# Performance work log

Hardware: AMD Instinct MI355X
Metric: run time of the kernel (lower is better)

## Reference

```python
import jax, jax.numpy as jnp
import numpy as np

BS, LATENT, HID, MAXLEN = 128, 512, 1024, 512

def setup_inputs() -> dict:
    key = jax.random.key(0)
    ks = jax.random.split(key, 12)
    s = 1.0 / np.sqrt(HID)  # pytorch default LSTM init scale
    inp = {}
    inp["decoder_input"] = jax.random.normal(ks[0], (BS, LATENT), jnp.float32)
    inp["lengths"] = jax.random.randint(ks[1], (BS,), 0, MAXLEN)
    # bidirectional single-layer LSTM params (gate order i,f,g,o; combined bias = b_ih+b_hh)
    inp["Wih_f"] = jax.random.uniform(ks[2], (4 * HID, LATENT), jnp.float32, -s, s)
    inp["Whh_f"] = jax.random.uniform(ks[3], (4 * HID, HID), jnp.float32, -s, s)
    inp["b_f"] = jax.random.uniform(ks[4], (4 * HID,), jnp.float32, -s, s)
    inp["Wih_b"] = jax.random.uniform(ks[5], (4 * HID, LATENT), jnp.float32, -s, s)
    inp["Whh_b"] = jax.random.uniform(ks[6], (4 * HID, HID), jnp.float32, -s, s)
    inp["b_b"] = jax.random.uniform(ks[7], (4 * HID,), jnp.float32, -s, s)
    # out: Linear(hidden -> latent); fc1: Linear(2*hidden -> 1)
    inp["W_out"] = jax.random.uniform(ks[8], (LATENT, HID), jnp.float32, -s, s)
    inp["b_out"] = jax.random.uniform(ks[9], (LATENT,), jnp.float32, -s, s)
    inp["W_fc1"] = jax.random.uniform(ks[10], (1, 2 * HID), jnp.float32, -s, s)
    inp["b_fc1"] = jax.random.uniform(ks[11], (1,), jnp.float32, -s, s)
    return inp

def _lstm_cell(x, h, c, Wih, Whh, b):
    z = x @ Wih.T + h @ Whh.T + b  # (bs, 4H)
    i, f, g, o = jnp.split(z, 4, axis=-1)
    c2 = jax.nn.sigmoid(f) * c + jax.nn.sigmoid(i) * jnp.tanh(g)
    h2 = jax.nn.sigmoid(o) * jnp.tanh(c2)
    return h2, c2

def reference(decoder_input, lengths, Wih_f, Whh_f, b_f, Wih_b, Whh_b, b_b,
              W_out, b_out, W_fc1, b_fc1):
    max_len = int(jnp.max(lengths))  # static decode length
    bs = decoder_input.shape[0]
    h0 = jnp.zeros((bs, HID), decoder_input.dtype)

    def step(carry, _):
        x, hf, cf, hb, cb = carry
        # bidirectional LSTM over a length-1 sequence = two cells on same input
        hf, cf = _lstm_cell(x, hf, cf, Wih_f, Whh_f, b_f)
        hb, cb = _lstm_cell(x, hb, cb, Wih_b, Whh_b, b_b)
        out_t = jnp.concatenate([hf, hb], axis=-1)  # (bs, 2H)
        # next input = out(h_n[-1]) i.e. backward-direction hidden
        x_next = hb @ W_out.T + b_out
        return (x_next, hf, cf, hb, cb), out_t

    carry0 = (decoder_input, h0, h0, h0, h0)
    _, outs = jax.lax.scan(step, carry0, xs=None, length=max_len)  # (T, bs, 2H)
    x = jnp.transpose(outs, (1, 0, 2))  # (bs, T, 2H)
    x = jax.nn.relu(x)
    return x @ W_fc1.T + b_fc1  # (bs, T, 1)
```

## Files before the change

kernel.cpp:

```cpp
#include <hip/hip_runtime.h>
#include <math.h>

typedef unsigned short u16;
typedef __attribute__((ext_vector_type(8))) short short8;
typedef __attribute__((ext_vector_type(4))) float f32x4;

__device__ __forceinline__ float sigm(float x) { return 1.0f / (1.0f + expf(-x)); }

__device__ __forceinline__ u16 f2bf(float x) {
    union { float f; unsigned u; } v; v.f = x;
    unsigned r = v.u + 0x7fffu + ((v.u >> 16) & 1u);
    return (u16)(r >> 16);
}
__device__ __forceinline__ float bf2f(u16 h) {
    union { unsigned u; float f; } v; v.u = ((unsigned)h) << 16;
    return v.f;
}
__device__ __forceinline__ f32x4 mfma16(short8 a, short8 b, f32x4 c) {
    return __builtin_amdgcn_mfma_f32_16x16x32_bf16(a, b, c, 0, 0, 0);
}
__device__ __forceinline__ void gl_lds16(const void* g, void* l) {
    __builtin_amdgcn_global_load_lds(
        (const __attribute__((address_space(1))) unsigned int*)g,
        (__attribute__((address_space(3))) unsigned int*)l, 16, 0, 0);
}
__device__ __forceinline__ int swz(int c) { return (c ^ (c >> 2)) & 3; }

__device__ __forceinline__ short8 ld_sc(const u16* p) {
    short8 r;
    asm volatile("global_load_dwordx4 %0, %1, off sc0 sc1"
                 : "=v"(r) : "v"(p) : "memory");
    return r;
}

__device__ __forceinline__ void grid_barrier(unsigned* cnt, unsigned* gen,
                                             unsigned nb, unsigned inst) {
    __syncthreads();
    if (threadIdx.x == 0) {
        const unsigned a = __hip_atomic_fetch_add(cnt, 1u, __ATOMIC_RELAXED,
                                                  __HIP_MEMORY_SCOPE_AGENT);
        if (a == nb * (inst + 1u) - 1u) {
            __hip_atomic_store(gen, inst + 1u, __ATOMIC_RELAXED,
                               __HIP_MEMORY_SCOPE_AGENT);
        } else {
            while (__hip_atomic_load(gen, __ATOMIC_RELAXED,
                                     __HIP_MEMORY_SCOPE_AGENT) < inst + 1u)
                __builtin_amdgcn_s_sleep(2);
        }
    }
    __syncthreads();
}

#define FENCE() asm volatile("" ::: "memory")

#define STAGE_W(kk, buf)                                                      \
    do {                                                                      \
        gl_lds16(Wsrc + sA + (kk), sm + (buf) * 8192 + lds0);                 \
        gl_lds16(Wsrc + sB + (kk), sm + (buf) * 8192 + lds1);                 \
    } while (0)

#define LOAD_A(kk, AH_, AL_)                                                  \
    do {                                                                      \
        _Pragma("unroll") for (int ks_ = 0; ks_ < 2; ++ks_) {                 \
            AH_[ks_] = ld_sc(Ah + aoff + (kk) + ks_ * 32);                    \
            AL_[ks_] = ld_sc(Al + aoff + (kk) + ks_ * 32);                    \
        }                                                                     \
    } while (0)

#define COMPUTE(bix, AH_, AL_, cix)                                           \
    do {                                                                      \
        const char* bb_ = sm + (bix) * 8192;                                  \
        _Pragma("unroll") for (int ks_ = 0; ks_ < 2; ++ks_) {                 \
            short8 bh_[2], bl_[2];                                            \
            _Pragma("unroll") for (int nt_ = 0; nt_ < 2; ++nt_) {             \
                const int col_ = nt_ * 16 + l15;                              \
                const int off_ = ks_ * 2048 + col_ * 64 + ((quad ^ swz(col_)) * 16); \
                bh_[nt_] = *(const short8*)(bb_ + off_);                      \
                bl_[nt_] = *(const short8*)(bb_ + 4096 + off_);               \
            }                                                                 \
            _Pragma("unroll") for (int nt_ = 0; nt_ < 2; ++nt_) {             \
                acc[nt_] = mfma16(AH_[ks_], bh_[nt_], acc[nt_]);              \
                acc[nt_] = mfma16(AL_[ks_], bh_[nt_], acc[nt_]);              \
                acc[nt_] = mfma16(AH_[ks_], bl_[nt_], acc[nt_]);              \
            }                                                                 \
        }                                                                     \
        if (fc1w) {                                                           \
            const int kb_ = (cix) * 64 + quad * 8;                            \
            _Pragma("unroll") for (int ks_ = 0; ks_ < 2; ++ks_) {             \
                const float* wp_ = smWf + kb_ + ks_ * 32;                     \
                const f32x4 w0_ = *(const f32x4*)(wp_);                       \
                const f32x4 w1_ = *(const f32x4*)(wp_ + 4);                   \
                const short8 hv_ = AH_[ks_];                                  \
                const short8 lv_ = AL_[ks_];                                  \
                _Pragma("unroll") for (int e_ = 0; e_ < 8; ++e_) {            \
                    const float v_ = bf2f((u16)hv_[e_]) + bf2f((u16)lv_[e_]); \
                    const float wv_ = (e_ < 4) ? w0_[e_] : w1_[e_ - 4];       \
                    fsum = fmaf(fmaxf(v_, 0.0f), wv_, fsum);                  \
                }                                                             \
            }                                                                 \
        }                                                                     \
    } while (0)

#define ITER(cc, BC, BS, AHU, ALU, AHL, ALL)                                  \
    do {                                                                      \
        asm volatile("s_waitcnt vmcnt(12)" ::: "memory");                     \
        __builtin_amdgcn_sched_barrier(0);                                    \
        __builtin_amdgcn_s_barrier();                                         \
        FENCE();                                                              \
        STAGE_W(((cc) + 3) * 64, BS);                                         \
        FENCE();                                                              \
        LOAD_A(((cc) + 3) * 64, AHL, ALL);                                    \
        COMPUTE(BC, AHU, ALU, (cc));                                          \
    } while (0)

__global__ __launch_bounds__(256, 2) void k_steps(
    u16* A0h, u16* A0l, u16* A1h, u16* A1l,
    const u16* __restrict__ WihH, const u16* __restrict__ WihL,
    const u16* __restrict__ WH, const u16* __restrict__ WL,
    const float* __restrict__ BR0, const float* __restrict__ BR1,
    const float* __restrict__ Wfc1, const float* __restrict__ bfc1,
    float* __restrict__ out,
    unsigned* barcnt, unsigned* bargen, int T)
{
    __shared__ __align__(16) char sm[32768];
    __shared__ __align__(16) char ze[9216];
    __shared__ __align__(16) float smWf[2048];

    const int tid = threadIdx.x, bid = blockIdx.x;
    const int w = tid >> 6, lane = tid & 63, l15 = lane & 15, quad = lane >> 4;
    const int dir = bid & 1;
    const int rest = bid >> 1;
    const int rowhalf = rest >> 7, colgrp = rest & 127;
    const int nbase = dir * 4096 + colgrp * 32;
    const int r0 = rowhalf * 64 + w * 16;
    const bool fc1b = (dir == 0) && (colgrp == 0);

    const int sp = w >> 1, skh = w & 1;
    const u16* Wsrc0 = sp ? WihL : WihH;
    const u16* WsrcN = sp ? WL : WH;
    size_t s0a, s0b, sNa, sNb;
    int lds0, lds1;
    {
        const int colA = 0 * 16 + (lane >> 2);
        const int colB = 1 * 16 + (lane >> 2);
        const int sa = (lane & 3) ^ swz(colA);
        const int sb = (lane & 3) ^ swz(colB);
        const size_t koffN = dir ? 1024 : 0;
        s0a = (size_t)(nbase + colA) * 512 + (size_t)(skh * 32 + sa * 8);
        s0b = (size_t)(nbase + colB) * 512 + (size_t)(skh * 32 + sb * 8);
        sNa = (size_t)(nbase + colA) * 2048 + koffN + (size_t)(skh * 32 + sa * 8);
        sNb = (size_t)(nbase + colB) * 2048 + koffN + (size_t)(skh * 32 + sb * 8);
        lds0 = sp * 4096 + skh * 2048;
        lds1 = lds0 + 1024;
    }

    const size_t abase = (size_t)(r0 + l15) * 2048 + (size_t)(quad * 8);
    const size_t aoffN = abase + (size_t)(dir ? 1024 : 0);

    const int ul = lane & 7;
    const f32x4 br0v = *(const f32x4*)(BR0 + nbase + ul * 4);
    const f32x4 br1v = *(const f32x4*)(BR1 + nbase + ul * 4);
    const float b1 = bfc1[0];
    float creg0 = 0.0f, creg1 = 0.0f;

    if (fc1b) {
        const f32x4 w0 = *(const f32x4*)(Wfc1 + tid * 8);
        const f32x4 w1 = *(const f32x4*)(Wfc1 + tid * 8 + 4);
        *(f32x4*)(smWf + tid * 8) = w0;
        *(f32x4*)(smWf + tid * 8 + 4) = w1;
    }
    asm volatile("s_waitcnt vmcnt(0) lgkmcnt(0)" ::: "memory");

    const unsigned nb = gridDim.x;

    for (int t = 0; t < T; ++t) {
        const int first = (t == 0);
        const u16* Ah = (t & 1) ? A1h : A0h;
        const u16* Al = (t & 1) ? A1l : A0l;
        u16* NAh = (t & 1) ? A0h : A1h;
        u16* NAl = (t & 1) ? A0l : A1l;
        const int nch = first ? 8 : (dir ? 16 : 32);
        const u16* Wsrc = first ? Wsrc0 : WsrcN;
        const size_t sA = first ? s0a : sNa;
        const size_t sB = first ? s0b : sNb;
        const size_t aoff = first ? abase : aoffN;
        const bool fc1w = fc1b && (t > 0);

        f32x4 acc[2] = {};
        short8 ah0[2], al0[2], ah1[2], al1[2];
        short8 ah2[2], al2[2], ah3[2], al3[2];
        float fsum = 0.0f;

        STAGE_W(0, 0);   FENCE(); LOAD_A(0, ah0, al0);   FENCE();
        STAGE_W(64, 1);  FENCE(); LOAD_A(64, ah1, al1);  FENCE();
        STAGE_W(128, 2); FENCE(); LOAD_A(128, ah2, al2); FENCE();

        for (int c = 0; c < nch; c += 4) {
            ITER(c + 0, 0, 3, ah0, al0, ah3, al3);
            ITER(c + 1, 1, 0, ah1, al1, ah0, al0);
            ITER(c + 2, 2, 1, ah2, al2, ah1, al1);
            ITER(c + 3, 3, 2, ah3, al3, ah2, al2);
        }
        asm volatile("s_waitcnt vmcnt(0)" ::: "memory");

        if (fc1w) {
            float v = fsum;
            v += __shfl_xor(v, 16);
            v += __shfl_xor(v, 32);
            if (lane < 16)
                out[(size_t)(r0 + l15) * T + (t - 1)] = v + b1;
        }

        char* zb = ze + w * 2304;
#pragma unroll
        for (int nt = 0; nt < 2; ++nt)
#pragma unroll
            for (int r = 0; r < 4; ++r)
                *(float*)(zb + (quad * 4 + r) * 144 + (nt * 16 + l15) * 4) = acc[nt][r];

        const f32x4 bv = first ? br0v : br1v;
#pragma unroll
        for (int p2 = 0; p2 < 2; ++p2) {
            const int ml = p2 * 8 + (lane >> 3);
            const f32x4 z = *(const f32x4*)(zb + ml * 144 + ul * 16);
            const float zi = z[0] + bv[0], zf = z[1] + bv[1];
            const float zg = z[2] + bv[2], zo = z[3] + bv[3];
            const float cold = p2 ? creg1 : creg0;
            const float c2 = sigm(zf) * cold + sigm(zi) * tanhf(zg);
            const float h2 = sigm(zo) * tanhf(c2);
            if (p2) creg1 = c2; else creg0 = c2;
            const u16 hh = f2bf(h2);
            const u16 hl = f2bf(h2 - bf2f(hh));
            const unsigned ohh = __shfl_xor((unsigned)hh, 1);
            const unsigned ohl = __shfl_xor((unsigned)hl, 1);
            if (!(lane & 1)) {
                const int u = colgrp * 8 + ul;
                const int m = r0 + ml;
                const size_t hidx = (size_t)m * 2048 + dir * 1024 + u;
                __hip_atomic_store((unsigned*)(NAh + hidx),
                                   (unsigned)hh | (ohh << 16),
                                   __ATOMIC_RELAXED, __HIP_MEMORY_SCOPE_AGENT);
                __hip_atomic_store((unsigned*)(NAl + hidx),
                                   (unsigned)hl | (ohl << 16),
                                   __ATOMIC_RELAXED, __HIP_MEMORY_SCOPE_AGENT);
            }
        }

        if (t + 1 < T)
            grid_barrier(barcnt, bargen, nb, (unsigned)t);
    }
}

__global__ __launch_bounds__(256) void k_tail(
    const u16* __restrict__ Ah, const u16* __restrict__ Al,
    const float* __restrict__ Wfc1, const float* __restrict__ bfc1,
    float* __restrict__ out, int T)
{
    __shared__ float red[256];
    const int m = blockIdx.x, tid = threadIdx.x;
    const size_t base = (size_t)m * 2048 + tid * 8;
    const short8 hv = *(const short8*)(Ah + base);
    const short8 lv = *(const short8*)(Al + base);
    float s = 0.0f;
#pragma unroll
    for (int e = 0; e < 8; ++e) {
        const float v = bf2f((u16)hv[e]) + bf2f((u16)lv[e]);
        s = fmaf(fmaxf(v, 0.0f), Wfc1[tid * 8 + e], s);
    }
    red[tid] = s;
    __syncthreads();
    for (int off = 128; off > 0; off >>= 1) {
        if (tid < off) red[tid] += red[tid + off];
        __syncthreads();
    }
    if (tid == 0) out[(size_t)m * T + T - 1] = red[0] + bfc1[0];
}

__global__ __launch_bounds__(256, 1) void k_fold(
    const u16* __restrict__ AH, const u16* __restrict__ AL,
    const u16* __restrict__ BH, const u16* __restrict__ BL,
    const float* __restrict__ Whh_b,
    u16* __restrict__ WH, u16* __restrict__ WL)
{
    const int tid = threadIdx.x, bid = blockIdx.x;
    const int w = tid >> 6, lane = tid & 63, l15 = lane & 15, quad = lane >> 4;
    const int bm = bid >> 4, bn = bid & 15;
    const int ar0 = bm * 64 + (w & 1) * 32;
    const int br0 = bn * 64 + (w >> 1) * 32;
    f32x4 acc[2][2] = {};
    for (int k0 = 0; k0 < 512; k0 += 32) {
        short8 a_h[2], a_l[2], b_h[2], b_l[2];
#pragma unroll
        for (int mt = 0; mt < 2; ++mt) {
            const size_t o = (size_t)(ar0 + mt * 16 + l15) * 512 + k0 + quad * 8;
            a_h[mt] = *(const short8*)(AH + o);
            a_l[mt] = *(const short8*)(AL + o);
        }
#pragma unroll
        for (int nt = 0; nt < 2; ++nt) {
            const size_t o = (size_t)(br0 + nt * 16 + l15) * 512 + k0 + quad * 8;
            b_h[nt] = *(const short8*)(BH + o);
            b_l[nt] = *(const short8*)(BL + o);
        }
#pragma unroll
        for (int mt = 0; mt < 2; ++mt)
#pragma unroll
            for (int nt = 0; nt < 2; ++nt) {
                acc[mt][nt] = mfma16(a_h[mt], b_h[nt], acc[mt][nt]);
                acc[mt][nt] = mfma16(a_l[mt], b_h[nt], acc[mt][nt]);
                acc[mt][nt] = mfma16(a_h[mt], b_l[nt], acc[mt][nt]);
            }
    }
#pragma unroll
    for (int mt = 0; mt < 2; ++mt)
#pragma unroll
        for (int nt = 0; nt < 2; ++nt)
#pragma unroll
            for (int r = 0; r < 4; ++r) {
                const int row = ar0 + mt * 16 + quad * 4 + r;
                const int j = br0 + nt * 16 + l15;
                float v = acc[mt][nt][r];
                if (row >= 4096)
                    v += Whh_b[(size_t)((row & 3) * 1024 + ((row & 4095) >> 2)) * 1024 + j];
                const size_t d = (size_t)row * 2048 + 1024 + j;
                const u16 hh = f2bf(v);
                WH[d] = hh;
                WL[d] = f2bf(v - bf2f(hh));
            }
}

__global__ __launch_bounds__(256) void k_prep(
    const float* __restrict__ dec,
    const float* __restrict__ Wih_f, const float* __restrict__ Whh_f,
    const float* __restrict__ b_f, const float* __restrict__ Wih_b,
    const float* __restrict__ b_b, const float* __restrict__ W_out,
    const float* __restrict__ b_out, const float* __restrict__ b_fc1,
    u16* __restrict__ WihH, u16* __restrict__ WihL,
    u16* __restrict__ WoTH, u16* __restrict__ WoTL,
    float* __restrict__ BR0, float* __restrict__ BR1,
    u16* __restrict__ A0h, u16* __restrict__ A0l,
    u16* __restrict__ WH, u16* __restrict__ WL,
    float* __restrict__ out, int out_size)
{
    const int t = blockIdx.x * 256 + threadIdx.x;
    if (t < 524288) {
        const int colp = t >> 6, kb = (t & 63) * 8;
        const int dir = colp >> 12, u = (colp & 4095) >> 2, g = colp & 3;
        const float* src = (dir ? Wih_b : Wih_f) + (size_t)(g * 1024 + u) * 512 + kb;
        const size_t d = (size_t)colp * 512 + kb;
#pragma unroll
        for (int j = 0; j < 8; ++j) {
            const float v = src[j];
            const u16 hh = f2bf(v);
            WihH[d + j] = hh; WihL[d + j] = f2bf(v - bf2f(hh));
        }
    } else if (t < 589824) {
        const int i = t - 524288, jc = i >> 6, lb = (i & 63) * 8;
#pragma unroll
        for (int jj = 0; jj < 8; ++jj) {
            const float v = W_out[(size_t)(lb + jj) * 1024 + jc];
            const size_t d = (size_t)jc * 512 + lb + jj;
            const u16 hh = f2bf(v);
            WoTH[d] = hh; WoTL[d] = f2bf(v - bf2f(hh));
        }
    } else if (t < 598016) {
        const int colp = t - 589824;
        const int dir = colp >> 12, u = (colp & 4095) >> 2, g = colp & 3;
        const float* Wih = dir ? Wih_b : Wih_f;
        const float s = (dir ? b_b : b_f)[g * 1024 + u];
        BR0[colp] = s;
        float dot = 0.0f;
        for (int l = 0; l < 512; ++l)
            dot += Wih[(size_t)(g * 1024 + u) * 512 + l] * b_out[l];
        BR1[colp] = s + dot;
    } else if (t < 606208) {
        const int i = t - 598016, m = i >> 6, kb = (i & 63) * 8;
#pragma unroll
        for (int j = 0; j < 8; ++j) {
            const float v = dec[(size_t)m * 512 + kb + j];
            const size_t d = (size_t)m * 2048 + kb + j;
            const u16 hh = f2bf(v);
            A0h[d] = hh; A0l[d] = f2bf(v - bf2f(hh));
        }
    } else if (t < 614400) {
        const int base = (t - 606208) * 8;
        const float b0 = b_fc1[0];
#pragma unroll
        for (int j = 0; j < 8; ++j)
            if (base + j < out_size) out[base + j] = b0;
    } else {
        const int i = t - 614400, colp = i >> 7, kb = (i & 127) * 8;
        const int u = colp >> 2, g = colp & 3;
        const float* src = Whh_f + (size_t)(g * 1024 + u) * 1024 + kb;
        const size_t d = (size_t)colp * 2048 + kb;
#pragma unroll
        for (int j = 0; j < 8; ++j) {
            const float v = src[j];
            const u16 hh = f2bf(v);
            WH[d + j] = hh; WL[d + j] = f2bf(v - bf2f(hh));
        }
    }
}

extern "C" void kernel_launch(void* const* d_in, const int* in_sizes, int n_in,
                              void* d_out, int out_size, void* d_ws, size_t ws_size,
                              hipStream_t stream) {
    const float* dec   = (const float*)d_in[0];
    const float* Wih_f = (const float*)d_in[2];
    const float* Whh_f = (const float*)d_in[3];
    const float* b_f   = (const float*)d_in[4];
    const float* Wih_b = (const float*)d_in[5];
    const float* Whh_b = (const float*)d_in[6];
    const float* b_b   = (const float*)d_in[7];
    const float* W_out = (const float*)d_in[8];
    const float* b_out = (const float*)d_in[9];
    const float* W_fc1 = (const float*)d_in[10];
    const float* b_fc1 = (const float*)d_in[11];
    float* out = (float*)d_out;

    char* ws = (char*)d_ws;
    u16* WH    = (u16*)(ws);
    u16* WL    = (u16*)(ws + 33554432);
    u16* WihH  = (u16*)(ws + 67108864);
    u16* WihL  = (u16*)(ws + 75497472);
    u16* WoTH  = (u16*)(ws + 83886080);
    u16* WoTL  = (u16*)(ws + 84934656);
    u16* A0h   = (u16*)(ws + 85983232);
    u16* A0l   = (u16*)(ws + 86507520);
    u16* A1h   = (u16*)(ws + 87031808);
    u16* A1l   = (u16*)(ws + 87556096);
    float* BR0 = (float*)(ws + 89128960);
    float* BR1 = (float*)(ws + 89161728);
    unsigned* barcnt = (unsigned*)(ws + 89194496);
    unsigned* bargen = (unsigned*)(ws + 89194624);

    k_prep<<<4448, 256, 0, stream>>>(dec, Wih_f, Whh_f, b_f, Wih_b, b_b,
                                     W_out, b_out, b_fc1,
                                     WihH, WihL, WoTH, WoTL, BR0, BR1,
                                     A0h, A0l, WH, WL, out, out_size);
    k_fold<<<2048, 256, 0, stream>>>(WihH, WihL, WoTH, WoTL, Whh_b, WH, WL);
    hipMemsetAsync(ws + 89194496, 0, 256, stream);

    const int T = out_size / 128;
    k_steps<<<512, 256, 0, stream>>>(A0h, A0l, A1h, A1l,
                                     WihH, WihL, WH, WL,
                                     BR0, BR1, W_fc1, b_fc1, out,
                                     barcnt, bargen, T);
    k_tail<<<128, 256, 0, stream>>>((T & 1) ? A1h : A0h, (T & 1) ? A1l : A0l,
                                    W_fc1, b_fc1, out, T);
}
```

Baseline: 21.63 ms.

## Use hierarchical grid barrier and double the K-chunk per pipeline stage

Replaces the flat single-counter grid barrier with a two-level barrier: groups of 8 blocks count on their own counters, and one representative per group bumps a root counter. This is meant to reduce atomic contention across 512 blocks at every timestep. It also doubles the K chunk per pipeline stage from 64 to 128, which halves the number of iterations and barriers per step. In exchange the LDS buffers double to 64KB, which may limit occupancy to one block per CU where launch bounds assume two. The z scratch buffer now aliases the staging buffer, with an added barrier to protect it, and the fc1 weights are read straight from global memory.

```diff
diff --git a/kernel.cpp b/kernel.cpp
--- a/kernel.cpp
+++ b/kernel.cpp
@@ -33,20 +33,24 @@
     return r;
 }
 
-__device__ __forceinline__ void grid_barrier(unsigned* cnt, unsigned* gen,
-                                             unsigned nb, unsigned inst) {
+__device__ __forceinline__ void grid_barrier(char* base, unsigned inst) {
     __syncthreads();
     if (threadIdx.x == 0) {
-        const unsigned a = __hip_atomic_fetch_add(cnt, 1u, __ATOMIC_RELAXED,
+        unsigned* root = (unsigned*)(base);
+        unsigned* gen  = (unsigned*)(base + 128);
+        unsigned* grp  = (unsigned*)(base + 256 + (blockIdx.x >> 3) * 128);
+        const unsigned a = __hip_atomic_fetch_add(grp, 1u, __ATOMIC_RELAXED,
                                                   __HIP_MEMORY_SCOPE_AGENT);
-        if (a == nb * (inst + 1u) - 1u) {
-            __hip_atomic_store(gen, inst + 1u, __ATOMIC_RELAXED,
-                               __HIP_MEMORY_SCOPE_AGENT);
-        } else {
-            while (__hip_atomic_load(gen, __ATOMIC_RELAXED,
-                                     __HIP_MEMORY_SCOPE_AGENT) < inst + 1u)
-                __builtin_amdgcn_s_sleep(2);
-        }
+        if (a == 8u * (inst + 1u) - 1u) {
+            const unsigned r = __hip_atomic_fetch_add(root, 1u, __ATOMIC_RELAXED,
+                                                      __HIP_MEMORY_SCOPE_AGENT);
+            if (r == 64u * (inst + 1u) - 1u)
+                __hip_atomic_store(gen, inst + 1u, __ATOMIC_RELAXED,
+                                   __HIP_MEMORY_SCOPE_AGENT);
+        }
+        while (__hip_atomic_load(gen, __ATOMIC_RELAXED,
+                                 __HIP_MEMORY_SCOPE_AGENT) < inst + 1u)
+            __builtin_amdgcn_s_sleep(2);
     }
     __syncthreads();
 }
@@ -55,43 +59,48 @@
 
 #define STAGE_W(kk, buf)                                                      \
     do {                                                                      \
-        gl_lds16(Wsrc + sA + (kk), sm + (buf) * 8192 + lds0);                 \
-        gl_lds16(Wsrc + sB + (kk), sm + (buf) * 8192 + lds1);                 \
+        _Pragma("unroll") for (int k64_ = 0; k64_ < 2; ++k64_) {              \
+            gl_lds16(Wsrc + sA + (kk) + k64_ * 64,                            \
+                     sm + (buf) * 16384 + ldsA + k64_ * 4096);                \
+            gl_lds16(Wsrc + sB + (kk) + k64_ * 64,                            \
+                     sm + (buf) * 16384 + ldsB + k64_ * 4096);                \
+        }                                                                     \
     } while (0)
 
 #define LOAD_A(kk, AH_, AL_)                                                  \
     do {                                                                      \
-        _Pragma("unroll") for (int ks_ = 0; ks_ < 2; ++ks_) {                 \
-            AH_[ks_] = ld_sc(Ah + aoff + (kk) + ks_ * 32);                    \
-            AL_[ks_] = ld_sc(Al + aoff + (kk) + ks_ * 32);                    \
+        _Pragma("unroll") for (int sb_ = 0; sb_ < 4; ++sb_) {                 \
+            AH_[sb_] = ld_sc(Ah + aoff + (kk) + sb_ * 32);                    \
+            AL_[sb_] = ld_sc(Al + aoff + (kk) + sb_ * 32);                    \
         }                                                                     \
     } while (0)
 
 #define COMPUTE(bix, AH_, AL_, cix)                                           \
     do {                                                                      \
-        const char* bb_ = sm + (bix) * 8192;                                  \
-        _Pragma("unroll") for (int ks_ = 0; ks_ < 2; ++ks_) {                 \
+        const char* bb_ = sm + (bix) * 16384;                                 \
+        _Pragma("unroll") for (int sb_ = 0; sb_ < 4; ++sb_) {                 \
+            const int k64_ = sb_ >> 1, ks_ = sb_ & 1;                         \
             short8 bh_[2], bl_[2];                                            \
             _Pragma("unroll") for (int nt_ = 0; nt_ < 2; ++nt_) {             \
                 const int col_ = nt_ * 16 + l15;                              \
-                const int off_ = ks_ * 2048 + col_ * 64 + ((quad ^ swz(col_)) * 16); \
+                const int off_ = k64_ * 4096 + ks_ * 2048 + col_ * 64 +       \
+                                 ((quad ^ swz(col_)) * 16);                   \
                 bh_[nt_] = *(const short8*)(bb_ + off_);                      \
-                bl_[nt_] = *(const short8*)(bb_ + 4096 + off_);               \
+                bl_[nt_] = *(const short8*)(bb_ + 8192 + off_);               \
             }                                                                 \
             _Pragma("unroll") for (int nt_ = 0; nt_ < 2; ++nt_) {             \
-                acc[nt_] = mfma16(AH_[ks_], bh_[nt_], acc[nt_]);              \
-                acc[nt_] = mfma16(AL_[ks_], bh_[nt_], acc[nt_]);              \
-                acc[nt_] = mfma16(AH_[ks_], bl_[nt_], acc[nt_]);              \
+                acc[nt_] = mfma16(AH_[sb_], bh_[nt_], acc[nt_]);              \
+                acc[nt_] = mfma16(AL_[sb_], bh_[nt_], acc[nt_]);              \
+                acc[nt_] = mfma16(AH_[sb_], bl_[nt_], acc[nt_]);              \
             }                                                                 \
         }                                                                     \
         if (fc1w) {                                                           \
-            const int kb_ = (cix) * 64 + quad * 8;                            \
-            _Pragma("unroll") for (int ks_ = 0; ks_ < 2; ++ks_) {             \
-                const float* wp_ = smWf + kb_ + ks_ * 32;                     \
+            _Pragma("unroll") for (int sb_ = 0; sb_ < 4; ++sb_) {             \
+                const float* wp_ = Wfc1 + (cix) * 128 + sb_ * 32 + quad * 8;  \
                 const f32x4 w0_ = *(const f32x4*)(wp_);                       \
                 const f32x4 w1_ = *(const f32x4*)(wp_ + 4);                   \
-                const short8 hv_ = AH_[ks_];                                  \
-                const short8 lv_ = AL_[ks_];                                  \
+                const short8 hv_ = AH_[sb_];                                  \
+                const short8 lv_ = AL_[sb_];                                  \
                 _Pragma("unroll") for (int e_ = 0; e_ < 8; ++e_) {            \
                     const float v_ = bf2f((u16)hv_[e_]) + bf2f((u16)lv_[e_]); \
                     const float wv_ = (e_ < 4) ? w0_[e_] : w1_[e_ - 4];       \
@@ -103,13 +112,13 @@
 
 #define ITER(cc, BC, BS, AHU, ALU, AHL, ALL)                                  \
     do {                                                                      \
-        asm volatile("s_waitcnt vmcnt(12)" ::: "memory");                     \
+        asm volatile("s_waitcnt vmcnt(24)" ::: "memory");                     \
         __builtin_amdgcn_sched_barrier(0);                                    \
         __builtin_amdgcn_s_barrier();                                         \
         FENCE();                                                              \
-        STAGE_W(((cc) + 3) * 64, BS);                                         \
+        STAGE_W(((cc) + 3) * 128, BS);                                        \
         FENCE();                                                              \
-        LOAD_A(((cc) + 3) * 64, AHL, ALL);                                    \
+        LOAD_A(((cc) + 3) * 128, AHL, ALL);                                   \
         COMPUTE(BC, AHU, ALU, (cc));                                          \
     } while (0)
 
@@ -119,12 +128,9 @@
     const u16* __restrict__ WH, const u16* __restrict__ WL,
     const float* __restrict__ BR0, const float* __restrict__ BR1,
     const float* __restrict__ Wfc1, const float* __restrict__ bfc1,
-    float* __restrict__ out,
-    unsigned* barcnt, unsigned* bargen, int T)
+    float* __restrict__ out, char* barbase, int T)
 {
-    __shared__ __align__(16) char sm[32768];
-    __shared__ __align__(16) char ze[9216];
-    __shared__ __align__(16) float smWf[2048];
+    __shared__ __align__(16) char sm[65536];
 
     const int tid = threadIdx.x, bid = blockIdx.x;
     const int w = tid >> 6, lane = tid & 63, l15 = lane & 15, quad = lane >> 4;
@@ -139,7 +145,7 @@
     const u16* Wsrc0 = sp ? WihL : WihH;
     const u16* WsrcN = sp ? WL : WH;
     size_t s0a, s0b, sNa, sNb;
-    int lds0, lds1;
+    int ldsA, ldsB;
     {
         const int colA = 0 * 16 + (lane >> 2);
         const int colB = 1 * 16 + (lane >> 2);
@@ -150,8 +156,8 @@
         s0b = (size_t)(nbase + colB) * 512 + (size_t)(skh * 32 + sb * 8);
         sNa = (size_t)(nbase + colA) * 2048 + koffN + (size_t)(skh * 32 + sa * 8);
         sNb = (size_t)(nbase + colB) * 2048 + koffN + (size_t)(skh * 32 + sb * 8);
-        lds0 = sp * 4096 + skh * 2048;
-        lds1 = lds0 + 1024;
+        ldsA = sp * 8192 + skh * 2048;
+        ldsB = ldsA + 1024;
     }
 
     const size_t abase = (size_t)(r0 + l15) * 2048 + (size_t)(quad * 8);
@@ -163,15 +169,7 @@
     const float b1 = bfc1[0];
     float creg0 = 0.0f, creg1 = 0.0f;
 
-    if (fc1b) {
-        const f32x4 w0 = *(const f32x4*)(Wfc1 + tid * 8);
-        const f32x4 w1 = *(const f32x4*)(Wfc1 + tid * 8 + 4);
-        *(f32x4*)(smWf + tid * 8) = w0;
-        *(f32x4*)(smWf + tid * 8 + 4) = w1;
-    }
     asm volatile("s_waitcnt vmcnt(0) lgkmcnt(0)" ::: "memory");
-
-    const unsigned nb = gridDim.x;
 
     for (int t = 0; t < T; ++t) {
         const int first = (t == 0);
@@ -179,7 +177,7 @@
         const u16* Al = (t & 1) ? A1l : A0l;
         u16* NAh = (t & 1) ? A0h : A1h;
         u16* NAl = (t & 1) ? A0l : A1l;
-        const int nch = first ? 8 : (dir ? 16 : 32);
+        const int nch = first ? 4 : (dir ? 8 : 16);
         const u16* Wsrc = first ? Wsrc0 : WsrcN;
         const size_t sA = first ? s0a : sNa;
         const size_t sB = first ? s0b : sNb;
@@ -187,13 +185,13 @@
         const bool fc1w = fc1b && (t > 0);
 
         f32x4 acc[2] = {};
-        short8 ah0[2], al0[2], ah1[2], al1[2];
-        short8 ah2[2], al2[2], ah3[2], al3[2];
+        short8 ah0[4], al0[4], ah1[4], al1[4];
+        short8 ah2[4], al2[4], ah3[4], al3[4];
         float fsum = 0.0f;
 
         STAGE_W(0, 0);   FENCE(); LOAD_A(0, ah0, al0);   FENCE();
-        STAGE_W(64, 1);  FENCE(); LOAD_A(64, ah1, al1);  FENCE();
-        STAGE_W(128, 2); FENCE(); LOAD_A(128, ah2, al2); FENCE();
+        STAGE_W(128, 1); FENCE(); LOAD_A(128, ah1, al1); FENCE();
+        STAGE_W(256, 2); FENCE(); LOAD_A(256, ah2, al2); FENCE();
 
         for (int c = 0; c < nch; c += 4) {
             ITER(c + 0, 0, 3, ah0, al0, ah3, al3);
@@ -202,6 +200,7 @@
             ITER(c + 3, 3, 2, ah3, al3, ah2, al2);
         }
         asm volatile("s_waitcnt vmcnt(0)" ::: "memory");
+        __builtin_amdgcn_s_barrier();
 
         if (fc1w) {
             float v = fsum;
@@ -211,7 +210,7 @@
                 out[(size_t)(r0 + l15) * T + (t - 1)] = v + b1;
         }
 
-        char* zb = ze + w * 2304;
+        char* zb = sm + w * 2304;
 #pragma unroll
         for (int nt = 0; nt < 2; ++nt)
 #pragma unroll
@@ -247,7 +246,7 @@
         }
 
         if (t + 1 < T)
-            grid_barrier(barcnt, bargen, nb, (unsigned)t);
+            grid_barrier(barbase, (unsigned)t);
     }
 }
 
@@ -429,23 +428,22 @@
     u16* A0l   = (u16*)(ws + 86507520);
     u16* A1h   = (u16*)(ws + 87031808);
     u16* A1l   = (u16*)(ws + 87556096);
+    char* barbase = ws + 88080384;
     float* BR0 = (float*)(ws + 89128960);
     float* BR1 = (float*)(ws + 89161728);
-    unsigned* barcnt = (unsigned*)(ws + 89194496);
-    unsigned* bargen = (unsigned*)(ws + 89194624);
 
     k_prep<<<4448, 256, 0, stream>>>(dec, Wih_f, Whh_f, b_f, Wih_b, b_b,
                                      W_out, b_out, b_fc1,
                                      WihH, WihL, WoTH, WoTL, BR0, BR1,
                                      A0h, A0l, WH, WL, out, out_size);
     k_fold<<<2048, 256, 0, stream>>>(WihH, WihL, WoTH, WoTL, Whh_b, WH, WL);
-    hipMemsetAsync(ws + 89194496, 0, 256, stream);
+    hipMemsetAsync(barbase, 0, 16384, stream);
 
     const int T = out_size / 128;
     k_steps<<<512, 256, 0, stream>>>(A0h, A0l, A1h, A1l,
                                      WihH, WihL, WH, WL,
                                      BR0, BR1, W_fc1, b_fc1, out,
-                                     barcnt, bargen, T);
+                                     barbase, T);
     k_tail<<<128, 256, 0, stream>>>((T & 1) ? A1h : A0h, (T & 1) ? A1l : A0l,
                                     W_fc1, b_fc1, out, T);
 }
```

New measurement: 30.61 ms. 41.6% more time.
